# Kernel optimization log

Hardware: AMD Instinct MI355X
Metric: run time of the kernel (lower is better)

## Reference

```python
import jax, jax.numpy as jnp
import numpy as np

N_NODES = 50000
N_EDGES = 800000
F_IN = 128
F_OUT = 64


def setup_inputs() -> dict:
    key = jax.random.key(0)
    k_x, k_w, k_r, k_c, k_v = jax.random.split(key, 5)
    x = jax.random.normal(k_x, (N_NODES, F_IN), dtype=jnp.float32)
    weight = jax.random.normal(k_w, (F_IN, F_OUT), dtype=jnp.float32)
    edge_row = jnp.sort(jax.random.randint(k_r, (N_EDGES,), 0, N_NODES, dtype=jnp.int32))
    edge_col = jax.random.randint(k_c, (N_EDGES,), 0, N_NODES, dtype=jnp.int32)
    edge_val = jax.random.uniform(k_v, (N_EDGES,), dtype=jnp.float32)
    return {"x": x, "weight": weight, "edge_row": edge_row,
            "edge_col": edge_col, "edge_val": edge_val}


def reference(x, weight, edge_row, edge_col, edge_val):
    # pre_sup = dot(x, W)                      : [N, F_out] dense GEMM
    pre_sup = x @ weight
    # support @ pre_sup (sparse-dense matmul) via COO gather + segment sum:
    # out[r] = sum_{e: row[e]==r} val[e] * pre_sup[col[e]]
    msgs = edge_val[:, None] * pre_sup[edge_col]          # [E, F_out]
    out = jax.ops.segment_sum(msgs, edge_row, num_segments=N_NODES)
    # act = relu, no bias
    return jax.nn.relu(out)
```

## Files before the change

kernel.cpp:

```cpp
#include <hip/hip_runtime.h>
#include <hip/hip_bf16.h>

#define F_IN 128
#define F_OUT 64

typedef __attribute__((ext_vector_type(8))) short short8;
typedef __attribute__((ext_vector_type(4))) float f32x4;

__device__ __forceinline__ unsigned short f2bf_rne(float f) {
  unsigned int u = __builtin_bit_cast(unsigned int, f);
  u += 0x7fffu + ((u >> 16) & 1u);
  return (unsigned short)(u >> 16);
}
__device__ __forceinline__ float bfu2f(unsigned short u) {
  return __builtin_bit_cast(float, (unsigned int)u << 16);
}
__device__ __forceinline__ float bf_lo(unsigned int u) {
  return __builtin_bit_cast(float, u << 16);
}
__device__ __forceinline__ float bf_hi(unsigned int u) {
  return __builtin_bit_cast(float, u & 0xffff0000u);
}

__global__ __launch_bounds__(256) void gcn_gemm_rowptr(
    const float* __restrict__ x, const float* __restrict__ w,
    unsigned short* __restrict__ pre,
    const int* __restrict__ edge_row, int* __restrict__ row_ptr,
    int n_nodes, int n_edges, int gemm_blocks) {
  const int tid = threadIdx.x;

  if (blockIdx.x >= gemm_blocks) {
    const int r = (blockIdx.x - gemm_blocks) * 256 + tid;
    if (r > n_nodes) return;
    int lo = 0, hi = n_edges;
    while (lo < hi) {
      const int mid = (lo + hi) >> 1;
      if (edge_row[mid] < r) lo = mid + 1; else hi = mid;
    }
    row_ptr[r] = lo;
    return;
  }

  __shared__ __align__(16) unsigned short wt_hi[64 * 128];

  {
#pragma unroll
    for (int i = 0; i < 8; ++i) {
      const int flat4 = tid + i * 256;
      const float4 v = ((const float4*)w)[flat4];
      const float fv[4] = {v.x, v.y, v.z, v.w};
#pragma unroll
      for (int j = 0; j < 4; ++j) {
        const int flat = flat4 * 4 + j;
        const int k = flat >> 6;
        const int n = flat & 63;
        int off = (n << 8) + (k << 1);
        off ^= (n & 7) << 4;
        *(unsigned short*)((char*)wt_hi + off) = f2bf_rne(fv[j]);
      }
    }
  }
  __syncthreads();

  const int lane = tid & 63;
  const int mt = blockIdx.x * 4 + (tid >> 6);
  const int m0 = mt * 16;
  if (m0 >= n_nodes) return;

  const int lrow = lane & 15;
  const int lk = lane >> 4;
  const bool full = (m0 + 16 <= n_nodes);
  const int arow = full ? (m0 + lrow) : min(m0 + lrow, n_nodes - 1);

  f32x4 acc[4];
#pragma unroll
  for (int i = 0; i < 4; ++i) acc[i] = (f32x4){0.f, 0.f, 0.f, 0.f};

#pragma unroll
  for (int ks = 0; ks < 4; ++ks) {
    const float4* xp =
        (const float4*)(x + (size_t)arow * F_IN + ks * 32 + lk * 8);
    const float4 q0 = xp[0];
    const float4 q1 = xp[1];
    const float fv[8] = {q0.x, q0.y, q0.z, q0.w, q1.x, q1.y, q1.z, q1.w};
    short8 ah, al;
#pragma unroll
    for (int i = 0; i < 8; ++i) {
      const unsigned short h = f2bf_rne(fv[i]);
      ah[i] = (short)h;
      al[i] = (short)f2bf_rne(fv[i] - bfu2f(h));
    }
#pragma unroll
    for (int nt = 0; nt < 4; ++nt) {
      const int n = nt * 16 + lrow;
      int off = (n << 8) + (ks * 64 + lk * 16);
      off ^= (n & 7) << 4;
      const short8 bh = *(const short8*)((const char*)wt_hi + off);
      acc[nt] = __builtin_amdgcn_mfma_f32_16x16x32_bf16(ah, bh, acc[nt], 0, 0, 0);
      acc[nt] = __builtin_amdgcn_mfma_f32_16x16x32_bf16(al, bh, acc[nt], 0, 0, 0);
    }
  }

#pragma unroll
  for (int nt = 0; nt < 4; ++nt) {
#pragma unroll
    for (int r = 0; r < 4; ++r) {
      const int row = m0 + lk * 4 + r;
      if (full || row < n_nodes)
        pre[(size_t)row * F_OUT + nt * 16 + lrow] = f2bf_rne(acc[nt][r]);
    }
  }
}

__global__ __launch_bounds__(256) void gcn_spmm(
    const unsigned short* __restrict__ pre, const int* __restrict__ row_ptr,
    const int* __restrict__ edge_col, const float* __restrict__ edge_val,
    float* __restrict__ out, int n_nodes) {
  const int lane = threadIdx.x & 63;
  const int half = lane >> 5;
  const int fl = lane & 31;
  int row = (int)((blockIdx.x * blockDim.x + threadIdx.x) >> 6);
  row = __builtin_amdgcn_readfirstlane(row);
  if (row >= n_nodes) return;
  const int e0 = row_ptr[row];
  const int e1 = row_ptr[row + 1];

  float a0 = 0.f, a1 = 0.f, a2 = 0.f, a3 = 0.f;
  const char* prebase = (const char*)pre + ((size_t)fl << 2);

  for (int base = e0; base < e1; base += 64) {
    const int cnt = min(64, e1 - base);
    int myc = 0;
    float myv = 0.f;
    if (lane < cnt) {
      myc = edge_col[base + lane] << 7;
      myv = edge_val[base + lane];
    }
    const int nb = (cnt + 15) >> 4;
    for (int b = 0; b < nb; ++b) {
      const int j0 = b * 16;
      int   cc[8];
      float vv[8];
#pragma unroll
      for (int j = 0; j < 8; ++j) {
        const int idx = j0 + j * 2 + half;
        cc[j] = __shfl(myc, idx);
        vv[j] = __shfl(myv, idx);
      }
      unsigned int p[8];
#pragma unroll
      for (int j = 0; j < 8; ++j)
        p[j] = *(const unsigned int*)(prebase + (size_t)(unsigned int)cc[j]);
#pragma unroll
      for (int j = 0; j < 8; j += 2) {
        a0 = fmaf(vv[j], bf_lo(p[j]), a0);
        a1 = fmaf(vv[j], bf_hi(p[j]), a1);
        a2 = fmaf(vv[j + 1], bf_lo(p[j + 1]), a2);
        a3 = fmaf(vv[j + 1], bf_hi(p[j + 1]), a3);
      }
    }
  }

  float s0 = (a0 + a2) + __shfl_xor(a0 + a2, 32);
  float s1 = (a1 + a3) + __shfl_xor(a1 + a3, 32);
  if (half == 0) {
    float2 o = make_float2(fmaxf(s0, 0.f), fmaxf(s1, 0.f));
    *(float2*)(out + (size_t)row * F_OUT + fl * 2) = o;
  }
}

extern "C" void kernel_launch(void* const* d_in, const int* in_sizes, int n_in,
                              void* d_out, int out_size, void* d_ws, size_t ws_size,
                              hipStream_t stream) {
  const float* x        = (const float*)d_in[0];
  const float* w        = (const float*)d_in[1];
  const int*   edge_row = (const int*)d_in[2];
  const int*   edge_col = (const int*)d_in[3];
  const float* edge_val = (const float*)d_in[4];
  float* out = (float*)d_out;

  const int n_nodes = in_sizes[0] / F_IN;
  const int n_edges = in_sizes[2];

  unsigned short* pre = (unsigned short*)d_ws;
  int* row_ptr = (int*)((char*)d_ws +
                        (size_t)n_nodes * F_OUT * sizeof(unsigned short));

  const int m_tiles = (n_nodes + 15) / 16;
  const int gemm_blocks = (m_tiles + 3) / 4;
  const int rp_blocks = (n_nodes + 1 + 255) / 256;
  gcn_gemm_rowptr<<<gemm_blocks + rp_blocks, 256, 0, stream>>>(
      x, w, pre, edge_row, row_ptr, n_nodes, n_edges, gemm_blocks);

  const int spmm_blocks = ((size_t)n_nodes * 64 + 255) / 256;
  gcn_spmm<<<spmm_blocks, 256, 0, stream>>>(pre, row_ptr, edge_col, edge_val,
                                            out, n_nodes);
}
```

Baseline: 32.56 us.

## Split pre-support into two feature planes and drop the low-part bf16 MFMA

The GEMM now converts x to a single bf16 term instead of a hi/lo split, which halves the MFMA work at reduced precision. The intermediate is stored as two 32-feature planes. The SpMM runs as two passes over blockIdx.y, each gathering 64-byte rows, with four edge groups per wave. This shrinks the gathered footprint per pass so it fits cache better. The cost is reading edge indices twice, doing two wave launches per row, and losing accuracy in the GEMM.

```diff
diff --git a/kernel.cpp b/kernel.cpp
--- a/kernel.cpp
+++ b/kernel.cpp
@@ -83,13 +83,9 @@
     const float4 q0 = xp[0];
     const float4 q1 = xp[1];
     const float fv[8] = {q0.x, q0.y, q0.z, q0.w, q1.x, q1.y, q1.z, q1.w};
-    short8 ah, al;
+    short8 ah;
 #pragma unroll
-    for (int i = 0; i < 8; ++i) {
-      const unsigned short h = f2bf_rne(fv[i]);
-      ah[i] = (short)h;
-      al[i] = (short)f2bf_rne(fv[i] - bfu2f(h));
-    }
+    for (int i = 0; i < 8; ++i) ah[i] = (short)f2bf_rne(fv[i]);
 #pragma unroll
     for (int nt = 0; nt < 4; ++nt) {
       const int n = nt * 16 + lrow;
@@ -97,17 +93,18 @@
       off ^= (n & 7) << 4;
       const short8 bh = *(const short8*)((const char*)wt_hi + off);
       acc[nt] = __builtin_amdgcn_mfma_f32_16x16x32_bf16(ah, bh, acc[nt], 0, 0, 0);
-      acc[nt] = __builtin_amdgcn_mfma_f32_16x16x32_bf16(al, bh, acc[nt], 0, 0, 0);
     }
   }
 
 #pragma unroll
   for (int nt = 0; nt < 4; ++nt) {
+    unsigned short* plane = pre + (size_t)(nt >> 1) * n_nodes * 32;
+    const int coff = (nt & 1) * 16 + lrow;
 #pragma unroll
     for (int r = 0; r < 4; ++r) {
       const int row = m0 + lk * 4 + r;
       if (full || row < n_nodes)
-        pre[(size_t)row * F_OUT + nt * 16 + lrow] = f2bf_rne(acc[nt][r]);
+        plane[(size_t)row * 32 + coff] = f2bf_rne(acc[nt][r]);
     }
   }
 }
@@ -117,55 +114,57 @@
     const int* __restrict__ edge_col, const float* __restrict__ edge_val,
     float* __restrict__ out, int n_nodes) {
   const int lane = threadIdx.x & 63;
-  const int half = lane >> 5;
-  const int fl = lane & 31;
+  const int q  = lane >> 4;
+  const int fl = lane & 15;
+  const int pass = blockIdx.y;
+  const unsigned short* plane = pre + (size_t)pass * n_nodes * 32;
+
   int row = (int)((blockIdx.x * blockDim.x + threadIdx.x) >> 6);
   row = __builtin_amdgcn_readfirstlane(row);
   if (row >= n_nodes) return;
   const int e0 = row_ptr[row];
   const int e1 = row_ptr[row + 1];
 
-  float a0 = 0.f, a1 = 0.f, a2 = 0.f, a3 = 0.f;
-  const char* prebase = (const char*)pre + ((size_t)fl << 2);
+  float a0 = 0.f, a1 = 0.f;
+  const char* prebase = (const char*)plane + ((size_t)fl << 2);
 
   for (int base = e0; base < e1; base += 64) {
     const int cnt = min(64, e1 - base);
     int myc = 0;
     float myv = 0.f;
     if (lane < cnt) {
-      myc = edge_col[base + lane] << 7;
+      myc = edge_col[base + lane] << 6;
       myv = edge_val[base + lane];
     }
-    const int nb = (cnt + 15) >> 4;
+    const int nb = (cnt + 31) >> 5;
     for (int b = 0; b < nb; ++b) {
-      const int j0 = b * 16;
+      const int j0 = b * 32;
       int   cc[8];
       float vv[8];
 #pragma unroll
-      for (int j = 0; j < 8; ++j) {
-        const int idx = j0 + j * 2 + half;
-        cc[j] = __shfl(myc, idx);
-        vv[j] = __shfl(myv, idx);
+      for (int g = 0; g < 8; ++g) {
+        const int idx = j0 + g * 4 + q;
+        cc[g] = __shfl(myc, idx);
+        vv[g] = __shfl(myv, idx);
       }
       unsigned int p[8];
 #pragma unroll
-      for (int j = 0; j < 8; ++j)
-        p[j] = *(const unsigned int*)(prebase + (size_t)(unsigned int)cc[j]);
+      for (int g = 0; g < 8; ++g)
+        p[g] = *(const unsigned int*)(prebase + (size_t)(unsigned int)cc[g]);
 #pragma unroll
-      for (int j = 0; j < 8; j += 2) {
-        a0 = fmaf(vv[j], bf_lo(p[j]), a0);
-        a1 = fmaf(vv[j], bf_hi(p[j]), a1);
-        a2 = fmaf(vv[j + 1], bf_lo(p[j + 1]), a2);
-        a3 = fmaf(vv[j + 1], bf_hi(p[j + 1]), a3);
+      for (int g = 0; g < 8; ++g) {
+        a0 = fmaf(vv[g], bf_lo(p[g]), a0);
+        a1 = fmaf(vv[g], bf_hi(p[g]), a1);
       }
     }
   }
 
-  float s0 = (a0 + a2) + __shfl_xor(a0 + a2, 32);
-  float s1 = (a1 + a3) + __shfl_xor(a1 + a3, 32);
-  if (half == 0) {
-    float2 o = make_float2(fmaxf(s0, 0.f), fmaxf(s1, 0.f));
-    *(float2*)(out + (size_t)row * F_OUT + fl * 2) = o;
+  a0 += __shfl_xor(a0, 16); a0 += __shfl_xor(a0, 32);
+  a1 += __shfl_xor(a1, 16); a1 += __shfl_xor(a1, 32);
+
+  if (q == 0) {
+    float2 o = make_float2(fmaxf(a0, 0.f), fmaxf(a1, 0.f));
+    *(float2*)(out + (size_t)row * F_OUT + pass * 32 + fl * 2) = o;
   }
 }
 
@@ -193,6 +192,6 @@
       x, w, pre, edge_row, row_ptr, n_nodes, n_edges, gemm_blocks);
 
   const int spmm_blocks = ((size_t)n_nodes * 64 + 255) / 256;
-  gcn_spmm<<<spmm_blocks, 256, 0, stream>>>(pre, row_ptr, edge_col, edge_val,
-                                            out, n_nodes);
+  gcn_spmm<<<dim3(spmm_blocks, 2), 256, 0, stream>>>(
+      pre, row_ptr, edge_col, edge_val, out, n_nodes);
 }
```

New measurement: 41.79 us. 28.4% more time.
